# Kernel tuning notes

Measured on AMD Instinct MI355X. Metric: run time of the kernel, lower is better.

The kernel has to match this reference:

```python
import jax, jax.numpy as jnp
import numpy as np

RMS_EPS = 1.1920929e-07  # torch.finfo(float32).eps, used by F.rms_norm default


def _rms_norm(x):
    # RMSNorm over last dim, no learnable weight (matches F.rms_norm(x, (d,)))
    ms = jnp.mean(jnp.square(x), axis=-1, keepdims=True)
    return x * jax.lax.rsqrt(ms + RMS_EPS)


def _apply_rotary(x, cos, sin):
    # x: [N, H, D]; cos/sin: [N, 1, D//2]
    d = x.shape[-1] // 2
    x1, x2 = x[..., :d], x[..., d:]
    y1 = x1 * cos + x2 * sin
    y2 = -x1 * sin + x2 * cos
    return jnp.concatenate([y1, y2], axis=-1)


def setup_inputs() -> dict:
    key = jax.random.key(0)
    k1, k2, k3 = jax.random.split(key, 3)
    n_embd, n_head, head_dim = 1024, 16, 64
    n_seqs, seqlen = 4, 1024
    N = n_seqs * seqlen
    x = jax.random.normal(k1, (N, n_embd), dtype=jnp.float32)
    Wqkv = jax.random.normal(k2, (3 * n_embd, n_embd), dtype=jnp.float32) * (n_embd ** -0.5)
    Wo = jax.random.normal(k3, (n_embd, n_embd), dtype=jnp.float32) * (n_embd ** -0.5)
    # standard rotary caches over positions [0, seqlen)
    inv_freq = 1.0 / (10000.0 ** (np.arange(0, head_dim // 2) / (head_dim // 2)))
    pos = np.arange(seqlen)[:, None] * inv_freq[None, :]  # [seqlen, head_dim//2]
    cos_cache = jnp.asarray(np.cos(pos), dtype=jnp.float32)
    sin_cache = jnp.asarray(np.sin(pos), dtype=jnp.float32)
    cu_seqlens = jnp.arange(n_seqs + 1, dtype=jnp.int32) * seqlen
    position_ids = jnp.tile(jnp.arange(seqlen, dtype=jnp.int32), n_seqs)
    return {"x": x, "Wqkv": Wqkv, "Wo": Wo, "cos_cache": cos_cache,
            "sin_cache": sin_cache, "cu_seqlens": cu_seqlens,
            "position_ids": position_ids, "max_seqlen": seqlen}


def reference(x, Wqkv, Wo, cos_cache, sin_cache, cu_seqlens, position_ids, max_seqlen):
    N, n_embd = x.shape
    S = int(max_seqlen)
    B = N // S  # equal-length packed sequences
    n_head = 16
    head_dim = n_embd // n_head

    qkv = (x @ Wqkv.T).reshape(N, 3, n_head, head_dim)
    cos = cos_cache[position_ids][:, None, :]  # [N,1,D/2]
    sin = sin_cache[position_ids][:, None, :]
    q = _rms_norm(_apply_rotary(qkv[:, 0], cos, sin))
    k = _rms_norm(_apply_rotary(qkv[:, 1], cos, sin))
    v = qkv[:, 2]

    q = q.reshape(B, S, n_head, head_dim)
    k = k.reshape(B, S, n_head, head_dim)
    v = v.reshape(B, S, n_head, head_dim)

    scale = head_dim ** -0.5
    scores = jnp.einsum('bqhd,bkhd->bhqk', q, k) * scale
    causal = jnp.tril(jnp.ones((S, S), dtype=bool))
    scores = jnp.where(causal, scores, jnp.finfo(scores.dtype).min)
    probs = jax.nn.softmax(scores, axis=-1)
    out = jnp.einsum('bhqk,bkhd->bqhd', probs, v).reshape(N, n_embd)
    return out @ Wo.T
```

## Files before the change

kernel.cpp:

```cpp
#include <hip/hip_runtime.h>
#include <hip/hip_bf16.h>

typedef unsigned short u16;
typedef __bf16 bf16x8 __attribute__((ext_vector_type(8)));
typedef float f32x4 __attribute__((ext_vector_type(4)));
typedef u16 u16x8 __attribute__((ext_vector_type(8)));
typedef u16 u16x4 __attribute__((ext_vector_type(4)));

__device__ __forceinline__ u16 f2bf(float f) {
    unsigned u = __builtin_bit_cast(unsigned, f);
    unsigned r = u + 0x7FFFu + ((u >> 16) & 1u);
    return (u16)(r >> 16);
}
__device__ __forceinline__ float bf2f(u16 h) {
    return __builtin_bit_cast(float, (unsigned)h << 16);
}
__device__ __forceinline__ unsigned cvt_pk_bf16(float lo, float hi) {
    unsigned r;
    asm("v_cvt_pk_bf16_f32 %0, %1, %2" : "=v"(r) : "v"(lo), "v"(hi));
    return r;
}
__device__ __forceinline__ void gload16(const void* g, void* l) {
    __builtin_amdgcn_global_load_lds((const __attribute__((address_space(1))) void*)g,
                                     (__attribute__((address_space(3))) void*)l, 16, 0, 0);
}

__global__ __launch_bounds__(256) void cvt_all(const float* __restrict__ x,
                                               const float* __restrict__ wqkv,
                                               const float* __restrict__ wo,
                                               u16* __restrict__ dst, int n0, int n1) {
    int i = (blockIdx.x * 256 + threadIdx.x) * 4;
    const float* src;
    if (i < n0)            src = x + i;
    else if (i < n0 + n1)  src = wqkv + (i - n0);
    else                   src = wo + (i - n0 - n1);
    float4 v = *(const float4*)src;
    u16x4 o;
    o[0] = f2bf(v.x); o[1] = f2bf(v.y); o[2] = f2bf(v.z); o[3] = f2bf(v.w);
    *(u16x4*)(dst + i) = o;
}

template <int BM, int BN, int WR, int WC, bool OUT_BF16, bool FUSE_ROPE>
__global__ __launch_bounds__(WR * WC * 64, (WR * WC == 8) ? 4 : 2)
void gemm_pipe(const u16* __restrict__ A,
               const u16* __restrict__ Bt,
               void* __restrict__ C,
               int M, int N, int K,
               const float* __restrict__ cosc,
               const float* __restrict__ sinc,
               const int* __restrict__ pos_ids,
               u16* __restrict__ vT, int S) {
    constexpr int NW = WR * WC;
    constexpr int MR = BM / WR / 16, NR = BN / WC / 16;
    constexpr int MGS = (MR >= 4) ? 4 : MR;
    constexpr int CA = BM / 8, CB = BN / 8;
    constexpr int CAW = CA / NW, CBW = CB / NW;
    constexpr int NLD = CAW + CBW;
    static_assert(!FUSE_ROPE || NR == 4, "FUSE_ROPE needs 64-col wave span");

    __shared__ u16 lA[2][BM * 64];
    __shared__ u16 lB[2][BN * 64];

    const int tid = threadIdx.x, lane = tid & 63, w = tid >> 6;
    const int wr = w / WC, wc = w % WC;
    const int lr = lane & 15, lg = lane >> 4;
    const int sw = (lr & 7) << 4;
    const int bm = blockIdx.x * BM, bn = blockIdx.y * BN;
    const int jr = lane >> 3;
    const int scbe = ((((lane & 7) * 16) ^ (jr << 4)) >> 1);
    const int nTk = K >> 6;

    f32x4 acc[MR][NR];
#pragma unroll
    for (int i = 0; i < MR; i++)
#pragma unroll
        for (int j = 0; j < NR; j++) acc[i][j] = (f32x4){0.f, 0.f, 0.f, 0.f};

    const u16* aSrc = A + (size_t)bm * K + scbe;
    const u16* bSrc = Bt + (size_t)bn * K + scbe;

#define STAGEP(p_, t_)                                                           \
    {                                                                            \
        _Pragma("unroll") for (int q = 0; q < CAW; q++) {                        \
            int ck = w * CAW + q;                                                \
            gload16(aSrc + (size_t)(ck * 8 + jr) * K + (t_) * 64,                \
                    &lA[p_][ck * 512]);                                          \
        }                                                                        \
        _Pragma("unroll") for (int q = 0; q < CBW; q++) {                        \
            int ck = w * CBW + q;                                                \
            gload16(bSrc + (size_t)(ck * 8 + jr) * K + (t_) * 64,                \
                    &lB[p_][ck * 512]);                                          \
        }                                                                        \
    }

    STAGEP(0, 0);

    for (int t = 0; t < nTk; t++) {
        const int p = t & 1;
        if (t + 1 < nTk) {
            STAGEP(p ^ 1, t + 1);
            if constexpr (NLD == 3)
                asm volatile("s_waitcnt vmcnt(3)" ::: "memory");
            else if constexpr (NLD == 4)
                asm volatile("s_waitcnt vmcnt(4)" ::: "memory");
            else if constexpr (NLD == 5)
                asm volatile("s_waitcnt vmcnt(5)" ::: "memory");
            else if constexpr (NLD == 6)
                asm volatile("s_waitcnt vmcnt(6)" ::: "memory");
            else if constexpr (NLD == 8)
                asm volatile("s_waitcnt vmcnt(8)" ::: "memory");
            else if constexpr (NLD == 10)
                asm volatile("s_waitcnt vmcnt(10)" ::: "memory");
            else
                asm volatile("s_waitcnt vmcnt(0)" ::: "memory");
        } else {
            asm volatile("s_waitcnt vmcnt(0)" ::: "memory");
        }
        __builtin_amdgcn_s_barrier();
        __builtin_amdgcn_sched_barrier(0);

        const char* pa = (const char*)&lA[p][0] + (size_t)(wr * MR * 16) * 128;
        const char* pb = (const char*)&lB[p][0] + (size_t)(wc * NR * 16) * 128;
#pragma unroll
        for (int ks = 0; ks < 2; ks++) {
            bf16x8 bfr[NR];
#pragma unroll
            for (int j = 0; j < NR; j++)
                bfr[j] = *(const bf16x8*)(pb + (j * 16 + lr) * 128 +
                                          ((ks * 64 + lg * 16) ^ sw));
#pragma unroll
            for (int mg = 0; mg < MR; mg += MGS) {
                bf16x8 af[MGS];
#pragma unroll
                for (int i = 0; i < MGS; i++)
                    af[i] = *(const bf16x8*)(pa + ((mg + i) * 16 + lr) * 128 +
                                             ((ks * 64 + lg * 16) ^ sw));
                __builtin_amdgcn_s_setprio(1);
#pragma unroll
                for (int i = 0; i < MGS; i++)
#pragma unroll
                    for (int j = 0; j < NR; j++)
                        acc[mg + i][j] = __builtin_amdgcn_mfma_f32_16x16x32_bf16(
                            af[i], bfr[j], acc[mg + i][j], 0, 0, 0);
                __builtin_amdgcn_s_setprio(0);
            }
        }
        __builtin_amdgcn_s_barrier();
    }
#undef STAGEP

    const int row0 = bm + wr * MR * 16, col0 = bn + wc * NR * 16;

    if constexpr (FUSE_ROPE) {
        u16* Cb = (u16*)C;
        if (col0 < 2048) {
            const float qs = (col0 < 1024) ? 0.18033688f : 1.0f;
#pragma unroll
            for (int i = 0; i < MR; i++) {
#pragma unroll
                for (int r = 0; r < 4; r++) {
                    const int m = row0 + i * 16 + lg * 4 + r;
                    const int pos = pos_ids[m];
                    const float c0 = cosc[pos * 32 + lr],      s0 = sinc[pos * 32 + lr];
                    const float c1 = cosc[pos * 32 + 16 + lr], s1 = sinc[pos * 32 + 16 + lr];
                    const float x0 = acc[i][0][r], x1 = acc[i][1][r];
                    const float x2 = acc[i][2][r], x3 = acc[i][3][r];
                    const float y0 = x0 * c0 + x2 * s0;
                    const float y2 = x2 * c0 - x0 * s0;
                    const float y1 = x1 * c1 + x3 * s1;
                    const float y3 = x3 * c1 - x1 * s1;
                    float ss = y0 * y0 + y1 * y1 + y2 * y2 + y3 * y3;
                    ss += __shfl_xor(ss, 1);
                    ss += __shfl_xor(ss, 2);
                    ss += __shfl_xor(ss, 4);
                    ss += __shfl_xor(ss, 8);
                    const float scl = rsqrtf(ss * (1.0f / 64.0f) + 1.1920929e-07f) * qs;
                    u16* cp = Cb + (size_t)m * N + col0 + lr;
                    cp[0]  = f2bf(y0 * scl);
                    cp[16] = f2bf(y1 * scl);
                    cp[32] = f2bf(y2 * scl);
                    cp[48] = f2bf(y3 * scl);
                }
            }
        } else {
            const int vcol = col0 - 2048;
            const int h = vcol >> 6;
            const int b = bm / S;
            const int s0 = row0 - b * S + lg * 4;
            u16* vbase = vT + ((size_t)(b * 16 + h) * 64) * S;
#pragma unroll
            for (int i = 0; i < MR; i++) {
                const int s = s0 + i * 16;
#pragma unroll
                for (int j = 0; j < NR; j++) {
                    const int d = j * 16 + lr;
                    u16x4 o;
#pragma unroll
                    for (int r = 0; r < 4; r++) o[r] = f2bf(acc[i][j][r]);
                    *(u16x4*)(vbase + (size_t)d * S + s) = o;
                }
            }
        }
        return;
    }

#pragma unroll
    for (int i = 0; i < MR; i++)
#pragma unroll
        for (int j = 0; j < NR; j++)
#pragma unroll
            for (int r = 0; r < 4; r++) {
                int m = row0 + i * 16 + lg * 4 + r;
                int n = col0 + j * 16 + lr;
                float v = acc[i][j][r];
                if (OUT_BF16)
                    ((u16*)C)[(size_t)m * N + n] = f2bf(v);
                else
                    ((float*)C)[(size_t)m * N + n] = v;
            }
}

__global__ __launch_bounds__(256) void attn_fwd(const u16* __restrict__ qkv,
                                                const u16* __restrict__ vT,
                                                u16* __restrict__ out, int S) {
    const int bh = blockIdx.x, b = bh >> 4, h = bh & 15;
    const int tid = threadIdx.x, lane = tid & 63, w = tid >> 6;
    const int lr = lane & 15, lg = lane >> 4;
    const int sw = (lr & 7) << 4;

    const int nq = S >> 6;
    const int i1 = blockIdx.y;
    const int i2 = (nq - 1) - i1;
    const int n1 = i1 + 1, ntot = n1 + i2 + 1;

    __shared__ u16 lK[3][64 * 64];
    __shared__ u16 lVt[3][64 * 64];
    __shared__ u16 lP[4][16 * 64];

    const int jr = lane >> 3;
    const int cbyte = (lane & 7) * 16;
    const int scb = cbyte ^ (jr << 4);
    const int rowA = w * 16 + jr, rowB = rowA + 8;
    const u16* kSrc = qkv + 1024 + h * 64 + (scb >> 1);
    const u16* vSrc = vT + (size_t)bh * 64 * S + (scb >> 1);

#define KVOF(x_) ((((x_) < n1) ? (x_) : (x_) - n1) * 64)

#define STAGE(bufi, kv0_)                                                        \
    {                                                                            \
        const u16* kb = kSrc + (size_t)(b * S + (kv0_)) * 3072;                  \
        const u16* vb = vSrc + (kv0_);                                           \
        gload16(kb + (size_t)rowA * 3072, &lK[bufi][(w * 2) * 512]);             \
        gload16(kb + (size_t)rowB * 3072, &lK[bufi][(w * 2 + 1) * 512]);         \
        gload16(vb + (size_t)rowA * S, &lVt[bufi][(w * 2) * 512]);               \
        gload16(vb + (size_t)rowB * S, &lVt[bufi][(w * 2 + 1) * 512]);           \
    }

    bf16x8 bQ[2];
    f32x4 oT[4];
    float lrun;

#define LOADQ(tile_)                                                             \
    {                                                                            \
        const u16* qp = qkv + (size_t)(b * S + (tile_)*64 + w * 16 + lr) * 3072 + h * 64; \
        bQ[0] = *(const bf16x8*)(qp + lg * 8);                                   \
        bQ[1] = *(const bf16x8*)(qp + 32 + lg * 8);                              \
    }

    STAGE(0, 0);
    if (1 < ntot) STAGE(1, KVOF(1));
    LOADQ(i1);
#pragma unroll
    for (int df = 0; df < 4; df++) oT[df] = (f32x4){0.f, 0.f, 0.f, 0.f};
    lrun = 0.f;

    int buf = 0;
    for (int s = 0; s < ntot; s++) {
        const int tile = (s < n1) ? i1 : i2;
        const int kv0 = KVOF(s);
        if (s + 1 < ntot)
            asm volatile("s_waitcnt vmcnt(4)" ::: "memory");
        else
            asm volatile("s_waitcnt vmcnt(0)" ::: "memory");
        __builtin_amdgcn_s_barrier();
        __builtin_amdgcn_sched_barrier(0);
        if (s + 2 < ntot) {
            int wb = buf + 2; if (wb >= 3) wb -= 3;
            STAGE(wb, KVOF(s + 2));
        }
        const bool diag = (s == n1 - 1) || (s == ntot - 1);

        f32x4 st[4];
#pragma unroll
        for (int kf = 0; kf < 4; kf++) {
            const char* kb = (const char*)&lK[buf][0] + (kf * 16 + lr) * 128;
            bf16x8 k0 = *(const bf16x8*)(kb + ((lg * 16) ^ sw));
            bf16x8 k1 = *(const bf16x8*)(kb + ((64 + lg * 16) ^ sw));
            f32x4 z = (f32x4){0.f, 0.f, 0.f, 0.f};
            z = __builtin_amdgcn_mfma_f32_16x16x32_bf16(k0, bQ[0], z, 0, 0, 0);
            st[kf] = __builtin_amdgcn_mfma_f32_16x16x32_bf16(k1, bQ[1], z, 0, 0, 0);
        }

        if (diag) {
            const int qg = tile * 64 + w * 16 + lr;
#pragma unroll
            for (int kf = 0; kf < 4; kf++)
#pragma unroll
                for (int r = 0; r < 4; r++) {
                    int kvg = kv0 + kf * 16 + lg * 4 + r;
                    if (kvg > qg) st[kf][r] = -3.0e38f;
                }
        }
        float ps = 0.f;
#pragma unroll
        for (int kf = 0; kf < 4; kf++)
#pragma unroll
            for (int r = 0; r < 4; r++) {
                float p = exp2f(st[kf][r]);
                st[kf][r] = p;
                ps += p;
            }
        lrun += ps;

        {
            char* pb = (char*)&lP[w][0] + lr * 128;
#pragma unroll
            for (int kf = 0; kf < 4; kf++) {
                uint2 pk;
                pk.x = cvt_pk_bf16(st[kf][0], st[kf][1]);
                pk.y = cvt_pk_bf16(st[kf][2], st[kf][3]);
                *(uint2*)(pb + ((kf * 32 + lg * 8) ^ sw)) = pk;
            }
        }

#pragma unroll
        for (int kc = 0; kc < 2; kc++) {
            bf16x8 bp = *(const bf16x8*)((const char*)&lP[w][0] + lr * 128 +
                                         ((kc * 64 + lg * 16) ^ sw));
#pragma unroll
            for (int df = 0; df < 4; df++) {
                bf16x8 av = *(const bf16x8*)((const char*)&lVt[buf][0] +
                                             (df * 16 + lr) * 128 +
                                             ((kc * 64 + lg * 16) ^ sw));
                oT[df] = __builtin_amdgcn_mfma_f32_16x16x32_bf16(av, bp, oT[df], 0, 0, 0);
            }
        }

        if (diag) {
            float tot = lrun;
            tot += __shfl_xor(tot, 16);
            tot += __shfl_xor(tot, 32);
            float inv = 1.0f / tot;
            u16* op = out + (size_t)(b * S + tile * 64 + w * 16 + lr) * 1024 +
                      h * 64 + lg * 4;
#pragma unroll
            for (int df = 0; df < 4; df++) {
                u16x4 o;
#pragma unroll
                for (int r = 0; r < 4; r++) o[r] = f2bf(oT[df][r] * inv);
                *(u16x4*)(op + df * 16) = o;
            }
            if (s != ntot - 1) {
                LOADQ(i2);
#pragma unroll
                for (int df = 0; df < 4; df++) oT[df] = (f32x4){0.f, 0.f, 0.f, 0.f};
                lrun = 0.f;
            }
        }
        buf++; if (buf == 3) buf = 0;
    }
#undef STAGE
#undef LOADQ
#undef KVOF
}

extern "C" void kernel_launch(void* const* d_in, const int* in_sizes, int n_in,
                              void* d_out, int out_size, void* d_ws, size_t ws_size,
                              hipStream_t stream) {
    const float* x     = (const float*)d_in[0];
    const float* Wqkv  = (const float*)d_in[1];
    const float* Wo    = (const float*)d_in[2];
    const float* cosc  = (const float*)d_in[3];
    const float* sinc  = (const float*)d_in[4];
    const int* pos_ids = (const int*)d_in[6];

    const int E = 1024, H = 16;
    int S = in_sizes[3] / 32;
    int N = in_sizes[0] / E;
    int B = N / S;

    char* ws = (char*)d_ws;
    u16* xb    = (u16*)ws;
    u16* wqkvb = (u16*)(ws + (size_t)N * E * 2);
    u16* wob   = (u16*)(ws + (size_t)N * E * 2 + (size_t)3 * E * E * 2);
    u16* qkvb  = (u16*)(ws + (size_t)N * E * 2 + (size_t)4 * E * E * 2);
    u16* vTb   = (u16*)(ws + (size_t)N * E * 2 + (size_t)4 * E * E * 2 + (size_t)N * 3 * E * 2);
    u16* aout  = xb;

    int n0 = N * E, n1 = 3 * E * E, n2 = E * E;
    cvt_all<<<(n0 + n1 + n2) / 1024, 256, 0, stream>>>(x, Wqkv, Wo, xb, n0, n1);

    gemm_pipe<128, 128, 4, 2, true, true><<<dim3(N / 128, 3 * E / 128), 512, 0, stream>>>(
        xb, wqkvb, qkvb, N, 3 * E, E, cosc, sinc, pos_ids, vTb, S);

    attn_fwd<<<dim3(B * H, S / 128), 256, 0, stream>>>(qkvb, vTb, aout, S);

    gemm_pipe<64, 128, 2, 4, false, false><<<dim3(N / 64, E / 128), 512, 0, stream>>>(
        aout, wob, d_out, N, E, E, nullptr, nullptr, nullptr, nullptr, 0);
}
```

Baseline: 93.80 us.

## Add triple-buffered LDS pipeline and shrink QKV GEMM row tile

Adds a DEPTH template parameter to the GEMM kernel. With DEPTH=3 it keeps two tiles of global-to-LDS loads in flight and needs only one barrier per k-step. The QKV projection GEMM now uses this 3-stage pipeline with a 64-row tile instead of 128, which doubles the number of blocks. The trade-off is that each wave holds only one MFMA row fragment, so operand reuse per wave drops, and LDS per block grows to about 74KB.

```diff
diff --git a/kernel.cpp b/kernel.cpp
--- a/kernel.cpp
+++ b/kernel.cpp
@@ -40,7 +40,7 @@
     *(u16x4*)(dst + i) = o;
 }
 
-template <int BM, int BN, int WR, int WC, bool OUT_BF16, bool FUSE_ROPE>
+template <int BM, int BN, int WR, int WC, bool OUT_BF16, bool FUSE_ROPE, int DEPTH>
 __global__ __launch_bounds__(WR * WC * 64, (WR * WC == 8) ? 4 : 2)
 void gemm_pipe(const u16* __restrict__ A,
                const u16* __restrict__ Bt,
@@ -58,8 +58,8 @@
     constexpr int NLD = CAW + CBW;
     static_assert(!FUSE_ROPE || NR == 4, "FUSE_ROPE needs 64-col wave span");
 
-    __shared__ u16 lA[2][BM * 64];
-    __shared__ u16 lB[2][BN * 64];
+    __shared__ u16 lA[DEPTH][BM * 64];
+    __shared__ u16 lB[DEPTH][BN * 64];
 
     const int tid = threadIdx.x, lane = tid & 63, w = tid >> 6;
     const int wr = w / WC, wc = w % WC;
@@ -93,61 +93,83 @@
         }                                                                        \
     }
 
-    STAGEP(0, 0);
-
-    for (int t = 0; t < nTk; t++) {
-        const int p = t & 1;
-        if (t + 1 < nTk) {
-            STAGEP(p ^ 1, t + 1);
-            if constexpr (NLD == 3)
-                asm volatile("s_waitcnt vmcnt(3)" ::: "memory");
-            else if constexpr (NLD == 4)
-                asm volatile("s_waitcnt vmcnt(4)" ::: "memory");
-            else if constexpr (NLD == 5)
-                asm volatile("s_waitcnt vmcnt(5)" ::: "memory");
-            else if constexpr (NLD == 6)
-                asm volatile("s_waitcnt vmcnt(6)" ::: "memory");
-            else if constexpr (NLD == 8)
-                asm volatile("s_waitcnt vmcnt(8)" ::: "memory");
-            else if constexpr (NLD == 10)
-                asm volatile("s_waitcnt vmcnt(10)" ::: "memory");
-            else
+#define WAIT_NLD()                                                               \
+    {                                                                            \
+        if constexpr (NLD == 2)                                                  \
+            asm volatile("s_waitcnt vmcnt(2)" ::: "memory");                     \
+        else if constexpr (NLD == 3)                                             \
+            asm volatile("s_waitcnt vmcnt(3)" ::: "memory");                     \
+        else if constexpr (NLD == 4)                                             \
+            asm volatile("s_waitcnt vmcnt(4)" ::: "memory");                     \
+        else if constexpr (NLD == 5)                                             \
+            asm volatile("s_waitcnt vmcnt(5)" ::: "memory");                     \
+        else if constexpr (NLD == 6)                                             \
+            asm volatile("s_waitcnt vmcnt(6)" ::: "memory");                     \
+        else if constexpr (NLD == 8)                                             \
+            asm volatile("s_waitcnt vmcnt(8)" ::: "memory");                     \
+        else                                                                     \
+            asm volatile("s_waitcnt vmcnt(0)" ::: "memory");                     \
+    }
+
+#define COMPUTE(p_)                                                              \
+    {                                                                            \
+        const char* pa = (const char*)&lA[p_][0] + (size_t)(wr * MR * 16) * 128; \
+        const char* pb = (const char*)&lB[p_][0] + (size_t)(wc * NR * 16) * 128; \
+        _Pragma("unroll") for (int ks = 0; ks < 2; ks++) {                       \
+            bf16x8 bfr[NR];                                                      \
+            _Pragma("unroll") for (int j = 0; j < NR; j++)                       \
+                bfr[j] = *(const bf16x8*)(pb + (j * 16 + lr) * 128 +             \
+                                          ((ks * 64 + lg * 16) ^ sw));           \
+            _Pragma("unroll") for (int mg = 0; mg < MR; mg += MGS) {             \
+                bf16x8 af[MGS];                                                  \
+                _Pragma("unroll") for (int i = 0; i < MGS; i++)                  \
+                    af[i] = *(const bf16x8*)(pa + ((mg + i) * 16 + lr) * 128 +   \
+                                             ((ks * 64 + lg * 16) ^ sw));        \
+                __builtin_amdgcn_s_setprio(1);                                   \
+                _Pragma("unroll") for (int i = 0; i < MGS; i++)                  \
+                    _Pragma("unroll") for (int j = 0; j < NR; j++)               \
+                        acc[mg + i][j] = __builtin_amdgcn_mfma_f32_16x16x32_bf16(\
+                            af[i], bfr[j], acc[mg + i][j], 0, 0, 0);             \
+                __builtin_amdgcn_s_setprio(0);                                   \
+            }                                                                    \
+        }                                                                        \
+    }
+
+    if constexpr (DEPTH == 3) {
+        STAGEP(0, 0);
+        if (1 < nTk) STAGEP(1, 1);
+        int p = 0;
+        for (int t = 0; t < nTk; t++) {
+            if (t + 1 < nTk) { WAIT_NLD(); }
+            else { asm volatile("s_waitcnt vmcnt(0)" ::: "memory"); }
+            __builtin_amdgcn_s_barrier();
+            __builtin_amdgcn_sched_barrier(0);
+            if (t + 2 < nTk) {
+                int wb = p + 2; if (wb >= 3) wb -= 3;
+                STAGEP(wb, t + 2);
+            }
+            COMPUTE(p);
+            p++; if (p == 3) p = 0;
+        }
+    } else {
+        STAGEP(0, 0);
+        for (int t = 0; t < nTk; t++) {
+            const int p = t & 1;
+            if (t + 1 < nTk) {
+                STAGEP(p ^ 1, t + 1);
+                WAIT_NLD();
+            } else {
                 asm volatile("s_waitcnt vmcnt(0)" ::: "memory");
-        } else {
-            asm volatile("s_waitcnt vmcnt(0)" ::: "memory");
-        }
-        __builtin_amdgcn_s_barrier();
-        __builtin_amdgcn_sched_barrier(0);
-
-        const char* pa = (const char*)&lA[p][0] + (size_t)(wr * MR * 16) * 128;
-        const char* pb = (const char*)&lB[p][0] + (size_t)(wc * NR * 16) * 128;
-#pragma unroll
-        for (int ks = 0; ks < 2; ks++) {
-            bf16x8 bfr[NR];
-#pragma unroll
-            for (int j = 0; j < NR; j++)
-                bfr[j] = *(const bf16x8*)(pb + (j * 16 + lr) * 128 +
-                                          ((ks * 64 + lg * 16) ^ sw));
-#pragma unroll
-            for (int mg = 0; mg < MR; mg += MGS) {
-                bf16x8 af[MGS];
-#pragma unroll
-                for (int i = 0; i < MGS; i++)
-                    af[i] = *(const bf16x8*)(pa + ((mg + i) * 16 + lr) * 128 +
-                                             ((ks * 64 + lg * 16) ^ sw));
-                __builtin_amdgcn_s_setprio(1);
-#pragma unroll
-                for (int i = 0; i < MGS; i++)
-#pragma unroll
-                    for (int j = 0; j < NR; j++)
-                        acc[mg + i][j] = __builtin_amdgcn_mfma_f32_16x16x32_bf16(
-                            af[i], bfr[j], acc[mg + i][j], 0, 0, 0);
-                __builtin_amdgcn_s_setprio(0);
-            }
-        }
-        __builtin_amdgcn_s_barrier();
+            }
+            __builtin_amdgcn_s_barrier();
+            __builtin_amdgcn_sched_barrier(0);
+            COMPUTE(p);
+            __builtin_amdgcn_s_barrier();
+        }
     }
 #undef STAGEP
+#undef WAIT_NLD
+#undef COMPUTE
 
     const int row0 = bm + wr * MR * 16, col0 = bn + wc * NR * 16;
 
@@ -400,11 +422,11 @@
     int n0 = N * E, n1 = 3 * E * E, n2 = E * E;
     cvt_all<<<(n0 + n1 + n2) / 1024, 256, 0, stream>>>(x, Wqkv, Wo, xb, n0, n1);
 
-    gemm_pipe<128, 128, 4, 2, true, true><<<dim3(N / 128, 3 * E / 128), 512, 0, stream>>>(
+    gemm_pipe<64, 128, 4, 2, true, true, 3><<<dim3(N / 64, 3 * E / 128), 512, 0, stream>>>(
         xb, wqkvb, qkvb, N, 3 * E, E, cosc, sinc, pos_ids, vTb, S);
 
     attn_fwd<<<dim3(B * H, S / 128), 256, 0, stream>>>(qkvb, vTb, aout, S);
 
-    gemm_pipe<64, 128, 2, 4, false, false><<<dim3(N / 64, E / 128), 512, 0, stream>>>(
+    gemm_pipe<64, 128, 2, 4, false, false, 2><<<dim3(N / 64, E / 128), 512, 0, stream>>>(
         aout, wob, d_out, N, E, E, nullptr, nullptr, nullptr, nullptr, 0);
 }
```

After: 101.6 us. 8.3% more time.
